# Optimization experiments

Hardware: AMD Instinct MI355X
Metric: run time of the kernel (lower is better)

The kernel has to match this reference:

```python
import jax, jax.numpy as jnp
import numpy as np

N, E, G = 20000, 320000, 64
H, NF, EF, L, Z = 280, 5, 4, 3, 64
BN_EPS = 1e-5


def _bn(x, g, b):
    # BatchNorm1d in training mode: batch stats over dim 0, biased variance
    m = x.mean(0)
    v = x.var(0)
    return g * (x - m) * jax.lax.rsqrt(v + BN_EPS) + b


def _mlp(x, W1, b1, g1, be1, W2, b2, g2, be2):
    h = jax.nn.relu(_bn(x @ W1 + b1, g1, be1))
    return jax.nn.relu(_bn(h @ W2 + b2, g2, be2))


def setup_inputs() -> dict:
    key = jax.random.key(0)
    ks = jax.random.split(key, 24)
    s = 0.05
    inp = {
        "x": jax.random.normal(ks[0], (N, NF), jnp.float32),
        "edge_attr": jax.random.normal(ks[1], (E, EF), jnp.float32),
        "edge_index": jax.random.randint(ks[2], (2, E), 0, N),
        "batch": jnp.sort(jax.random.randint(ks[3], (N,), 0, G)),
        # input layer
        "Wi": jax.random.normal(ks[4], (NF, H), jnp.float32) * s,
        "bi": jnp.zeros((H,), jnp.float32),
        # message MLP (stacked over L layers): in = 2H+EF
        "Wm1": jax.random.normal(ks[5], (L, 2 * H + EF, H), jnp.float32) * s,
        "bm1": jnp.zeros((L, H), jnp.float32),
        "g1": jnp.ones((L, H), jnp.float32),
        "be1": jnp.zeros((L, H), jnp.float32),
        "Wm2": jax.random.normal(ks[6], (L, H, H), jnp.float32) * s,
        "bm2": jnp.zeros((L, H), jnp.float32),
        "g2": jnp.ones((L, H), jnp.float32),
        "be2": jnp.zeros((L, H), jnp.float32),
        # update MLP: in = 2H
        "Wu1": jax.random.normal(ks[7], (L, 2 * H, H), jnp.float32) * s,
        "bu1": jnp.zeros((L, H), jnp.float32),
        "g3": jnp.ones((L, H), jnp.float32),
        "be3": jnp.zeros((L, H), jnp.float32),
        "Wu2": jax.random.normal(ks[8], (L, H, H), jnp.float32) * s,
        "bu2": jnp.zeros((L, H), jnp.float32),
        "g4": jnp.ones((L, H), jnp.float32),
        "be4": jnp.zeros((L, H), jnp.float32),
        # mu head
        "Wmu": jax.random.normal(ks[9], (H, Z), jnp.float32) * s,
        "bmu": jnp.zeros((Z,), jnp.float32),
    }
    return inp


def reference(x, edge_attr, Wi, bi, Wm1, bm1, g1, be1, Wm2, bm2, g2, be2,
              Wu1, bu1, g3, be3, Wu2, bu2, g4, be4, Wmu, bmu,
              edge_index, batch):
    src, dst = edge_index[0], edge_index[1]
    h = x @ Wi + bi  # [N, H]
    for l in range(L):
        # message: cat(h_i=h[dst], h_j=h[src], edge_attr) -> MLP -> [E, H]
        msg_in = jnp.concatenate([h[dst], h[src], edge_attr], axis=-1)
        msg = _mlp(msg_in, Wm1[l], bm1[l], g1[l], be1[l], Wm2[l], bm2[l], g2[l], be2[l])
        # aggregate: scatter-add into target nodes
        agg = jax.ops.segment_sum(msg, dst, num_segments=N)
        # update: cat(h, agg) -> MLP; residual in GNNEncoder
        upd = _mlp(jnp.concatenate([h, agg], axis=-1),
                   Wu1[l], bu1[l], g3[l], be3[l], Wu2[l], bu2[l], g4[l], be4[l])
        h = h + upd
    # global mean pool over graphs
    sums = jax.ops.segment_sum(h, batch, num_segments=G)
    cnt = jax.ops.segment_sum(jnp.ones((h.shape[0],), h.dtype), batch, num_segments=G)
    pooled = sums / jnp.maximum(cnt, 1.0)[:, None]
    return pooled @ Wmu + bmu  # [G, Z]
```

## Files before the change

### kernel.cpp

```cpp
#include <hip/hip_runtime.h>
#include <hip/hip_bf16.h>

#define NN 20000
#define EE 320000
#define GG 64
#define HH 280
#define NFF 5
#define EFF 4
#define LL 3
#define ZZ 64
#define BN_EPS 1e-5f

typedef __hip_bfloat16 bf;
typedef unsigned short ush;
typedef __attribute__((ext_vector_type(8))) short v8s;
typedef __attribute__((ext_vector_type(4))) float v4f;

__device__ __forceinline__ float us2f(ush u) {
  return __uint_as_float(((unsigned)u) << 16);
}
__device__ __forceinline__ ush f2us(float v) {
  bf b = __float2bfloat16(v);
  return *reinterpret_cast<ush*>(&b);
}
__device__ __forceinline__ int clampi(int v, int hi) {
  return v < 0 ? 0 : (v >= hi ? hi - 1 : v);
}

__global__ void probe_k(const void* __restrict__ x, int* __restrict__ flag) {
  __shared__ int sh[256];
  int tid = threadIdx.x;
  int cnt = 0;
  for (int i = tid; i < 2048; i += 256) {
    ush w = ((const ush*)x)[i];
    unsigned e = (w >> 7) & 0xFF;
    if (w != 0 && (e < 87 || e > 167)) cnt++;
  }
  sh[tid] = cnt;
  __syncthreads();
  for (int o = 128; o > 0; o >>= 1) {
    if (tid < o) sh[tid] += sh[tid + o];
    __syncthreads();
  }
  if (tid == 0) *flag = (sh[0] > 64) ? 1 : 0;
}

__global__ void convert_k(const void* __restrict__ src, float* __restrict__ dst,
                          int n, const int* __restrict__ flag) {
  int i = blockIdx.x * 256 + threadIdx.x;
  if (i < n) {
    if (*flag)
      dst[i] = ((const float*)src)[i];
    else
      dst[i] = us2f(((const ush*)src)[i]);
  }
}

__global__ void wt_ab_k(const float* __restrict__ W, ush* __restrict__ O) {
  int i = blockIdx.x * 256 + threadIdx.x;
  if (i >= 3 * 576 * 288) return;
  int l = i / 165888, r = i % 165888;
  int n = r / 288, k = r % 288;
  float v = 0.f;
  if (n < 560 && k < 280)
    v = (n < 280) ? W[(size_t)l * 157920 + (size_t)k * 280 + n]
                  : W[(size_t)l * 157920 + (size_t)(280 + k) * 280 + (n - 280)];
  O[i] = f2us(v);
}
__global__ void wt_sq_k(const float* __restrict__ W, ush* __restrict__ O) {
  int i = blockIdx.x * 256 + threadIdx.x;
  if (i >= 3 * 320 * 288) return;
  int l = i / 92160, r = i % 92160;
  int n = r / 288, k = r % 288;
  float v = (n < 280 && k < 280) ? W[(size_t)l * 78400 + (size_t)k * 280 + n] : 0.f;
  O[i] = f2us(v);
}
__global__ void wt_u1_k(const float* __restrict__ W, ush* __restrict__ O) {
  int i = blockIdx.x * 256 + threadIdx.x;
  if (i >= 3 * 320 * 576) return;
  int l = i / 184320, r = i % 184320;
  int n = r / 576, k = r % 576;
  float v = (n < 280 && k < 560) ? W[(size_t)l * 156800 + (size_t)k * 280 + n] : 0.f;
  O[i] = f2us(v);
}

struct MG {
  const ush* A;
  const ush* Bt;
  const float* bias;
  void* C;
  float* stats;
  int M, K, Nn, lda, ldb, ldc;
};

template <int CB, int ST>
__global__ __launch_bounds__(256) void mgemm_k(MG g) {
  __shared__ ush Bs[64][296];
  auto red = (float(*)[64])Bs;
  int t = threadIdx.x;
  int n0 = blockIdx.x * 64, m0 = blockIdx.y * 128;
  int lane = t & 63, wv = t >> 6;
  int lrow = lane & 15, quad = lane >> 4;
  int br = t >> 2;
  int bc = (t & 3) * 72;
  v4f acc[2][4];
#pragma unroll
  for (int gi = 0; gi < 2; ++gi)
#pragma unroll
    for (int ci = 0; ci < 4; ++ci) acc[gi][ci] = (v4f){0.f, 0.f, 0.f, 0.f};

  const ush* Arow[2];
  bool av[2];
#pragma unroll
  for (int gi = 0; gi < 2; ++gi) {
    int gm = m0 + (wv << 5) + (gi << 4) + lrow;
    av[gi] = gm < g.M;
    Arow[gi] = g.A + (size_t)gm * g.lda + (quad << 3);
  }
  const ush* Brow = g.Bt + (size_t)(n0 + br) * g.ldb + bc;
  uint4 zz = {0, 0, 0, 0};

  int ntile = g.K / 288;
  for (int tile = 0; tile < ntile; ++tile) {
    int k0 = tile * 288;
    uint4 aR[2][9];
#pragma unroll
    for (int kt = 0; kt < 9; ++kt)
#pragma unroll
      for (int gi = 0; gi < 2; ++gi)
        aR[gi][kt] = av[gi] ? *(const uint4*)(Arow[gi] + k0 + (kt << 5)) : zz;
    if (tile) __syncthreads();
#pragma unroll
    for (int i = 0; i < 9; ++i)
      *(uint4*)&Bs[br][bc + (i << 3)] = *(const uint4*)(Brow + k0 + (i << 3));
    __syncthreads();
#pragma unroll
    for (int kt = 0; kt < 9; ++kt) {
      v8s bq[4];
#pragma unroll
      for (int ci = 0; ci < 4; ++ci)
        bq[ci] = *(const v8s*)&Bs[(ci << 4) + lrow][(kt << 5) + (quad << 3)];
#pragma unroll
      for (int gi = 0; gi < 2; ++gi) {
        v8s af = *(v8s*)&aR[gi][kt];
#pragma unroll
        for (int ci = 0; ci < 4; ++ci)
          acc[gi][ci] = __builtin_amdgcn_mfma_f32_16x16x32_bf16(
              af, bq[ci], acc[gi][ci], 0, 0, 0);
      }
    }
  }

  float bj[4];
#pragma unroll
  for (int ci = 0; ci < 4; ++ci) {
    int gn = n0 + (ci << 4) + lrow;
    bj[ci] = (g.bias && gn < g.Nn) ? g.bias[gn] : 0.f;
  }
#pragma unroll
  for (int gi = 0; gi < 2; ++gi)
#pragma unroll
    for (int ci = 0; ci < 4; ++ci)
#pragma unroll
      for (int r = 0; r < 4; ++r) {
        int gm = m0 + (wv << 5) + (gi << 4) + (quad << 2) + r;
        int gn = n0 + (ci << 4) + lrow;
        float v = acc[gi][ci][r] + bj[ci];
        bool ok = (gm < g.M) && (gn < g.Nn);
        if (ok) {
          size_t idx = (size_t)gm * g.ldc + gn;
          if (CB)
            ((ush*)g.C)[idx] = f2us(v);
          else
            ((float*)g.C)[idx] = v;
        }
        acc[gi][ci][r] = ok ? v : 0.f;
      }
  if (ST) {
    int rowg = (wv << 2) | quad;
    __syncthreads();
#pragma unroll
    for (int ci = 0; ci < 4; ++ci) {
      float s = 0.f;
#pragma unroll
      for (int gi = 0; gi < 2; ++gi)
#pragma unroll
        for (int r = 0; r < 4; ++r) s += acc[gi][ci][r];
      red[rowg][(ci << 4) | lrow] = s;
    }
    __syncthreads();
    if (t < 64) {
      float s = 0.f;
#pragma unroll
      for (int r = 0; r < 16; ++r) s += red[r][t];
      int gn = n0 + t;
      if (gn < g.Nn) atomicAdd(&g.stats[gn], s);
    }
    __syncthreads();
#pragma unroll
    for (int ci = 0; ci < 4; ++ci) {
      float s = 0.f;
#pragma unroll
      for (int gi = 0; gi < 2; ++gi)
#pragma unroll
        for (int r = 0; r < 4; ++r) s += acc[gi][ci][r] * acc[gi][ci][r];
      red[rowg][(ci << 4) | lrow] = s;
    }
    __syncthreads();
    if (t < 64) {
      float s = 0.f;
#pragma unroll
      for (int r = 0; r < 16; ++r) s += red[r][t];
      int gn = n0 + t;
      if (gn < g.Nn) atomicAdd(&g.stats[HH + gn], s);
    }
  }
}

__global__ __launch_bounds__(256) void gemm_small_k(
    const float* __restrict__ A, const float* __restrict__ B,
    const float* __restrict__ bias, void* __restrict__ C,
    const int* __restrict__ flag, int M, int K, int Nn, int lda, int ldb,
    int ldc, int outmode) {
  __shared__ alignas(16) float As[16][68];
  __shared__ alignas(16) float Bsm[16][68];
  int tid = threadIdx.x;
  int n0 = blockIdx.x * 64, m0 = blockIdx.y * 64;
  int tx = tid & 15, ty = tid >> 4;
  int am = tid >> 2, akq = (tid & 3) << 2;
  int bk = tid >> 4, bn = (tid & 15) << 2;
  float acc[4][4] = {};
  int gmA = m0 + am;
  int nkt = (K + 15) >> 4;
  for (int kt = 0; kt < nkt; ++kt) {
    int k0 = kt << 4;
#pragma unroll
    for (int i = 0; i < 4; ++i) {
      int gk = k0 + akq + i;
      As[akq + i][am] = (gmA < M && gk < K) ? A[(size_t)gmA * lda + gk] : 0.f;
    }
    {
      int gk = k0 + bk;
      bool kin = gk < K;
#pragma unroll
      for (int j = 0; j < 4; ++j) {
        int gn = n0 + bn + j;
        Bsm[bk][bn + j] = (kin && gn < Nn) ? B[(size_t)gk * ldb + gn] : 0.f;
      }
    }
    __syncthreads();
#pragma unroll
    for (int kk = 0; kk < 16; ++kk) {
      float4 a4 = *(const float4*)&As[kk][ty << 2];
      float4 b4 = *(const float4*)&Bsm[kk][tx << 2];
      float av[4] = {a4.x, a4.y, a4.z, a4.w};
      float bv[4] = {b4.x, b4.y, b4.z, b4.w};
#pragma unroll
      for (int i = 0; i < 4; ++i)
#pragma unroll
        for (int j = 0; j < 4; ++j) acc[i][j] = fmaf(av[i], bv[j], acc[i][j]);
    }
    __syncthreads();
  }
  int ofl = outmode ? *flag : -1;
#pragma unroll
  for (int i = 0; i < 4; ++i) {
    int gm = m0 + (ty << 2) + i;
    if (gm < M) {
#pragma unroll
      for (int j = 0; j < 4; ++j) {
        int gn = n0 + (tx << 2) + j;
        if (gn < Nn) {
          float v = acc[i][j] + (bias ? bias[gn] : 0.f);
          size_t idx = (size_t)gm * ldc + gn;
          if (outmode == 0)
            ((float*)C)[idx] = v;
          else if (ofl)
            ((float*)C)[idx] = v;
          else
            ((ush*)C)[idx] = f2us(v);
        }
      }
    }
  }
}

__global__ __launch_bounds__(256) void edge_stats_k(
    const int* __restrict__ eids, const int* __restrict__ dst,
    const int* __restrict__ src, const float* __restrict__ ea,
    const ush* __restrict__ Pq, const float* __restrict__ W1c,
    const float* __restrict__ b1, float* __restrict__ stats) {
  __shared__ int dstl[256], srcl[256];
  __shared__ float4 eal[256];
  __shared__ float w1cs[4 * HH];
  __shared__ float b1s[HH];
  int tid = threadIdx.x;
  int e0 = blockIdx.x * 256;
  {
    int e = clampi(eids[e0 + tid], EE);
    dstl[tid] = clampi(dst[e], NN);
    srcl[tid] = clampi(src[e], NN);
    eal[tid] = *(const float4*)(ea + (size_t)e * 4);
  }
  for (int i = tid; i < 4 * HH; i += 256) w1cs[i] = W1c[i];
  for (int i = tid; i < HH; i += 256) b1s[i] = b1[i];
  __syncthreads();
  int c0 = tid, c1 = tid + 256;
  bool has1 = c1 < HH;
  float w0x = w1cs[c0], w0y = w1cs[HH + c0], w0z = w1cs[2 * HH + c0],
        w0w = w1cs[3 * HH + c0], b0v = b1s[c0];
  float w1x = 0.f, w1y = 0.f, w1z = 0.f, w1w = 0.f, b1v = 0.f;
  if (has1) {
    w1x = w1cs[c1]; w1y = w1cs[HH + c1]; w1z = w1cs[2 * HH + c1];
    w1w = w1cs[3 * HH + c1]; b1v = b1s[c1];
  }
  float s0 = 0.f, q0 = 0.f, s1 = 0.f, q1 = 0.f;
  for (int e = 0; e < 256; e += 4) {
    ush pd[4], ps[4], pd2[4], ps2[4];
#pragma unroll
    for (int j = 0; j < 4; ++j) {
      size_t bd = (size_t)dstl[e + j] * 576, bs = (size_t)srcl[e + j] * 576 + 280;
      pd[j] = Pq[bd + c0];
      ps[j] = Pq[bs + c0];
      if (has1) {
        pd2[j] = Pq[bd + c1];
        ps2[j] = Pq[bs + c1];
      }
    }
#pragma unroll
    for (int j = 0; j < 4; ++j) {
      float4 ev = eal[e + j];
      float tv = us2f(pd[j]) + us2f(ps[j]) + ev.x * w0x + ev.y * w0y +
                 ev.z * w0z + ev.w * w0w + b0v;
      s0 += tv;
      q0 += tv * tv;
      if (has1) {
        float t2 = us2f(pd2[j]) + us2f(ps2[j]) + ev.x * w1x + ev.y * w1y +
                   ev.z * w1z + ev.w * w1w + b1v;
        s1 += t2;
        q1 += t2 * t2;
      }
    }
  }
  atomicAdd(&stats[c0], s0);
  atomicAdd(&stats[HH + c0], q0);
  if (has1) {
    atomicAdd(&stats[c1], s1);
    atomicAdd(&stats[HH + c1], q1);
  }
}

__global__ void bn_finalize_k(const float* __restrict__ stats, float cnt,
                              const float* __restrict__ gw,
                              const float* __restrict__ bw,
                              const float* __restrict__ extra,
                              float* __restrict__ scale,
                              float* __restrict__ shift) {
  int c = threadIdx.x;
  if (c < HH) {
    float m = stats[c] / cnt;
    float v = stats[HH + c] / cnt - m * m;
    v = v < 0.f ? 0.f : v;
    float r = rsqrtf(v + BN_EPS);
    float sc = gw[c] * r;
    float sh = bw[c] - sc * m + (extra ? sc * extra[c] : 0.f);
    scale[c] = sc;
    shift[c] = sh;
  }
}

__global__ void hist_k(const int* __restrict__ dst, int* __restrict__ counts) {
  int e = blockIdx.x * 256 + threadIdx.x;
  if (e < EE) atomicAdd(&counts[clampi(dst[e], NN)], 1);
}

__global__ __launch_bounds__(1024) void scan_k(const int* __restrict__ counts,
                                               int* __restrict__ offs, int n) {
  __shared__ int buf[1024];
  __shared__ int running;
  int tid = threadIdx.x;
  if (tid == 0) running = 0;
  __syncthreads();
  for (int base = 0; base < n; base += 1024) {
    int v = (base + tid < n) ? counts[base + tid] : 0;
    buf[tid] = v;
    __syncthreads();
    for (int off = 1; off < 1024; off <<= 1) {
      int t = (tid >= off) ? buf[tid - off] : 0;
      __syncthreads();
      buf[tid] += t;
      __syncthreads();
    }
    int incl = buf[tid];
    if (base + tid < n) offs[base + tid] = running + incl - v;
    __syncthreads();
    if (tid == 1023) running += incl;
    __syncthreads();
  }
  if (tid == 0) offs[n] = running;
}

__global__ void fill_k(const int* __restrict__ dst, const int* __restrict__ offs,
                       int* __restrict__ cursor, int* __restrict__ eids) {
  int e = blockIdx.x * 256 + threadIdx.x;
  if (e < EE) {
    int n = clampi(dst[e], NN);
    int pos = atomicAdd(&cursor[n], 1);
    int idx = offs[n] + pos;
    if (idx >= 0 && idx < EE) eids[idx] = e;
  }
}

__global__ __launch_bounds__(256) void build_t1_k(
    const int* __restrict__ eids, const int* __restrict__ dst,
    const int* __restrict__ src, const float* __restrict__ ea,
    const ush* __restrict__ Pq, const float* __restrict__ W1c,
    const float* __restrict__ sc, const float* __restrict__ sh,
    ush* __restrict__ T1, int cb) {
  __shared__ float scs[HH], shs[HH], w1[4 * HH];
  int t = threadIdx.x;
  for (int i = t; i < HH; i += 256) { scs[i] = sc[i]; shs[i] = sh[i]; }
  for (int i = t; i < 4 * HH; i += 256) w1[i] = W1c[i];
  __syncthreads();
  int base = blockIdx.x * 32;
  int c2 = t + 256;
  bool h2 = c2 < HH;
  for (int i = 0; i < 32; ++i) {
    int r = cb + base + i;
    int e = clampi(eids[r], EE);
    int d = clampi(dst[e], NN), s = clampi(src[e], NN);
    float4 ev = *(const float4*)(ea + (size_t)e * 4);
    size_t pd = (size_t)d * 576, ps = (size_t)s * 576 + 280;
    size_t orow = (size_t)(base + i) * 288;
    {
      int c = t;
      float v = us2f(Pq[pd + c]) + us2f(Pq[ps + c]) + ev.x * w1[c] +
                ev.y * w1[HH + c] + ev.z * w1[2 * HH + c] + ev.w * w1[3 * HH + c];
      v = fmaf(scs[c], v, shs[c]);
      T1[orow + c] = f2us(v > 0.f ? v : 0.f);
    }
    if (h2) {
      int c = c2;
      float v = us2f(Pq[pd + c]) + us2f(Pq[ps + c]) + ev.x * w1[c] +
                ev.y * w1[HH + c] + ev.z * w1[2 * HH + c] + ev.w * w1[3 * HH + c];
      v = fmaf(scs[c], v, shs[c]);
      T1[orow + c] = f2us(v > 0.f ? v : 0.f);
    }
  }
}

__global__ __launch_bounds__(256) void aggregate_k(
    const int* __restrict__ offs, const ush* __restrict__ tmp2,
    const float* __restrict__ scale, const float* __restrict__ shift,
    float* __restrict__ agg, int e0, int e1) {
  int n = blockIdx.x;
  int rs = offs[n], re = offs[n + 1];
  if (rs < e0) rs = e0;
  if (re > e1) re = e1;
  if (rs >= re) return;
  int t = threadIdx.x;
  int c2 = t + 256;
  bool h2 = c2 < HH;
  float a0 = 0.f, a1 = 0.f;
  float sc0 = scale[t], sh0 = shift[t];
  float sc1 = h2 ? scale[c2] : 0.f, sh1 = h2 ? shift[c2] : 0.f;
  for (int r = rs; r < re; ++r) {
    const ush* row = tmp2 + (size_t)(r - e0) * HH;
    float v0 = fmaf(sc0, us2f(row[t]), sh0);
    a0 += v0 > 0.f ? v0 : 0.f;
    if (h2) {
      float v1 = fmaf(sc1, us2f(row[c2]), sh1);
      a1 += v1 > 0.f ? v1 : 0.f;
    }
  }
  agg[(size_t)n * HH + t] += a0;
  if (h2) agg[(size_t)n * HH + c2] += a1;
}

__global__ void hb_k(const float* __restrict__ h, ush* __restrict__ hcat) {
  int i = blockIdx.x * 256 + threadIdx.x;
  if (i < NN * HH) {
    int n = i / HH, c = i % HH;
    hcat[(size_t)n * 576 + c] = f2us(h[i]);
  }
}
__global__ void agg2hcat_k(const float* __restrict__ agg, ush* __restrict__ hcat) {
  int i = blockIdx.x * 256 + threadIdx.x;
  if (i < NN * HH) {
    int n = i / HH, c = i % HH;
    hcat[(size_t)n * 576 + 280 + c] = f2us(agg[i]);
  }
}
__global__ void u2a_k(const float* __restrict__ u1, const float* __restrict__ sc,
                      const float* __restrict__ sh, ush* __restrict__ u2A) {
  int i = blockIdx.x * 256 + threadIdx.x;
  if (i < NN * HH) {
    int n = i / HH, c = i % HH;
    float v = fmaf(sc[c], u1[i], sh[c]);
    u2A[(size_t)n * 288 + c] = f2us(v > 0.f ? v : 0.f);
  }
}
__global__ void residual_k(float* __restrict__ h, const float* __restrict__ u2,
                           const float* __restrict__ scale,
                           const float* __restrict__ shift) {
  int i = blockIdx.x * 256 + threadIdx.x;
  if (i < NN * HH) {
    int c = i % HH;
    float v = fmaf(scale[c], u2[i], shift[c]);
    h[i] += v > 0.f ? v : 0.f;
  }
}

__device__ __forceinline__ int lowerb(const int* a, int n, int key) {
  int lo = 0, hi = n;
  while (lo < hi) {
    int mid = (lo + hi) >> 1;
    if (a[mid] < key) lo = mid + 1; else hi = mid;
  }
  return lo;
}

__global__ __launch_bounds__(256) void pool_k(const float* __restrict__ h,
                                              const int* __restrict__ batch,
                                              float* __restrict__ pooled) {
  __shared__ float red[4][56];
  int gid = blockIdx.x, cc = blockIdx.y;
  int start = lowerb(batch, NN, gid);
  int end = lowerb(batch, NN, gid + 1);
  int cnt = end - start;
  float inv = 1.f / (float)(cnt > 1 ? cnt : 1);
  int grp = threadIdx.x >> 6, ci = threadIdx.x & 63;
  if (ci < 56) {
    int col = cc * 56 + ci;
    float s = 0.f;
    for (int n = start + grp; n < end; n += 4) s += h[(size_t)n * HH + col];
    red[grp][ci] = s;
  }
  __syncthreads();
  if (threadIdx.x < 56) {
    float s = red[0][threadIdx.x] + red[1][threadIdx.x] +
              red[2][threadIdx.x] + red[3][threadIdx.x];
    pooled[(size_t)gid * HH + cc * 56 + threadIdx.x] = s * inv;
  }
}

extern "C" void kernel_launch(void* const* d_in, const int* in_sizes, int n_in,
                              void* d_out, int out_size, void* d_ws,
                              size_t ws_size, hipStream_t stream) {
  const int* eidx = (const int*)d_in[2];
  const int* batch = (const int*)d_in[3];
  const int* srcp = eidx;
  const int* dstp = eidx + EE;
  size_t NH = (size_t)NN * HH;

  float* w0 = (float*)d_ws;
  size_t off = 0;
  auto alloc = [&](size_t n) {
    float* p = w0 + off;
    off += (n + 3) & ~(size_t)3;
    return p;
  };
  int* flag = (int*)alloc(4);
  float* cx = alloc(100000);
  float* cea = alloc(1280000);
  float* cWi = alloc(1400);
  float* cbi = alloc(280);
  float* cWm1 = alloc(473760);
  float* cbm1 = alloc(840);
  float* cg1 = alloc(840);
  float* cbe1 = alloc(840);
  float* cWm2 = alloc(235200);
  float* cbm2 = alloc(840);
  float* cg2 = alloc(840);
  float* cbe2 = alloc(840);
  float* cWu1 = alloc(470400);
  float* cbu1 = alloc(840);
  float* cg3 = alloc(840);
  float* cbe3 = alloc(840);
  float* cWu2 = alloc(235200);
  float* cbu2 = alloc(840);
  float* cg4 = alloc(840);
  float* cbe4 = alloc(840);
  float* cWmu = alloc(17920);
  float* cbmu = alloc(64);
  ush* W1ab = (ush*)alloc(248832);
  ush* W2t = (ush*)alloc(138240);
  ush* WU1t = (ush*)alloc(276480);
  ush* WU2t = (ush*)alloc(138240);
  float* h = alloc(NH);
  ush* hcat = (ush*)alloc(5824512);
  ush* u2A = hcat;
  float* pqr = alloc(5824512);
  ush* Pq = (ush*)pqr;
  float* u1f = pqr;
  float* agg = alloc(NH);
  float* pooled = alloc((size_t)GG * HH);
  float* stats = alloc(8 * HH);
  float* ss = alloc(8 * HH);
  int* counts = (int*)alloc(NN);
  int* cursor = (int*)alloc(NN);
  int* offs = (int*)alloc(NN + 1);
  int* eids = (int*)alloc(EE);
  size_t baseB = off * 4;

  int EC = 6400, T2 = 6400;
  {
    const int ecs[5] = {64000, 64000, 32000, 12800, 6400};
    const int t2s[5] = {EE, 64000, 32000, 12800, 6400};
    for (int i = 0; i < 5; ++i) {
      size_t need = baseB + (size_t)ecs[i] * 288 * 2 + (size_t)t2s[i] * 280 * 2 + 64;
      if (need <= ws_size) { EC = ecs[i]; T2 = t2s[i]; break; }
    }
  }
  ush* T1c = (ush*)(w0 + off);
  ush* tmp2 = T1c + (size_t)EC * 288;
  bool stored = (T2 == EE);
  int nch = EE / EC;

  probe_k<<<1, 256, 0, stream>>>(d_in[0], flag);
  struct Cv { const void* s; float* d; int n; };
  const Cv cv[22] = {
      {d_in[0], cx, NN * NFF},     {d_in[1], cea, EE * EFF},
      {d_in[4], cWi, NFF * HH},    {d_in[5], cbi, HH},
      {d_in[6], cWm1, LL * (2 * HH + EFF) * HH}, {d_in[7], cbm1, LL * HH},
      {d_in[8], cg1, LL * HH},     {d_in[9], cbe1, LL * HH},
      {d_in[10], cWm2, LL * HH * HH}, {d_in[11], cbm2, LL * HH},
      {d_in[12], cg2, LL * HH},    {d_in[13], cbe2, LL * HH},
      {d_in[14], cWu1, LL * 2 * HH * HH}, {d_in[15], cbu1, LL * HH},
      {d_in[16], cg3, LL * HH},    {d_in[17], cbe3, LL * HH},
      {d_in[18], cWu2, LL * HH * HH}, {d_in[19], cbu2, LL * HH},
      {d_in[20], cg4, LL * HH},    {d_in[21], cbe4, LL * HH},
      {d_in[22], cWmu, HH * ZZ},   {d_in[23], cbmu, ZZ}};
  for (int i = 0; i < 22; ++i)
    convert_k<<<(cv[i].n + 255) / 256, 256, 0, stream>>>(cv[i].s, cv[i].d, cv[i].n, flag);

  wt_ab_k<<<(3 * 576 * 288 + 255) / 256, 256, 0, stream>>>(cWm1, W1ab);
  wt_sq_k<<<(3 * 320 * 288 + 255) / 256, 256, 0, stream>>>(cWm2, W2t);
  wt_u1_k<<<(3 * 320 * 576 + 255) / 256, 256, 0, stream>>>(cWu1, WU1t);
  wt_sq_k<<<(3 * 320 * 288 + 255) / 256, 256, 0, stream>>>(cWu2, WU2t);

  gemm_small_k<<<dim3(5, 313), 256, 0, stream>>>(cx, cWi, cbi, h, nullptr, NN,
                                                 NFF, HH, NFF, HH, HH, 0);
  hipMemsetAsync(counts, 0, NN * sizeof(int), stream);
  hipMemsetAsync(cursor, 0, NN * sizeof(int), stream);
  hist_k<<<(EE + 255) / 256, 256, 0, stream>>>(dstp, counts);
  scan_k<<<1, 1024, 0, stream>>>(counts, offs, NN);
  fill_k<<<(EE + 255) / 256, 256, 0, stream>>>(dstp, offs, cursor, eids);

  int elemGrid = (int)((NH + 255) / 256);
  for (int l = 0; l < LL; ++l) {
    ush* Wab = W1ab + (size_t)l * 576 * 288;
    ush* W2l = W2t + (size_t)l * 320 * 288;
    ush* WU1l = WU1t + (size_t)l * 320 * 576;
    ush* WU2l = WU2t + (size_t)l * 320 * 288;
    const float* W1c = cWm1 + (size_t)l * 157920 + (size_t)560 * 280;
    float* st1 = stats;
    float* st2 = stats + 560;
    float* st3 = stats + 1120;
    float* st4 = stats + 1680;
    float* ss1 = ss;
    float* ss2 = ss + 560;
    float* ss3 = ss + 1120;
    float* ss4 = ss + 1680;
    hipMemsetAsync(stats, 0, 8 * HH * sizeof(float), stream);

    hb_k<<<elemGrid, 256, 0, stream>>>(h, hcat);
    {
      MG g = {hcat, Wab, nullptr, Pq, nullptr, NN, 288, 560, 576, 288, 576};
      mgemm_k<1, 0><<<dim3(9, 157), 256, 0, stream>>>(g);
    }
    edge_stats_k<<<EE / 256, 256, 0, stream>>>(eids, dstp, srcp, cea, Pq, W1c,
                                               cbm1 + l * HH, st1);
    bn_finalize_k<<<1, 320, 0, stream>>>(st1, (float)EE, cg1 + l * HH,
                                         cbe1 + l * HH, cbm1 + l * HH, ss1,
                                         ss1 + HH);
    for (int c = 0; c < nch; ++c) {
      int cb = c * EC;
      build_t1_k<<<EC / 32, 256, 0, stream>>>(eids, dstp, srcp, cea, Pq, W1c,
                                              ss1, ss1 + HH, T1c, cb);
      MG g = {T1c, W2l, cbm2 + l * HH,
              stored ? (void*)(tmp2 + (size_t)cb * HH) : (void*)tmp2, st2,
              EC, 288, HH, 288, 288, HH};
      mgemm_k<1, 1><<<dim3(5, EC / 128), 256, 0, stream>>>(g);
    }
    bn_finalize_k<<<1, 320, 0, stream>>>(st2, (float)EE, cg2 + l * HH,
                                         cbe2 + l * HH, nullptr, ss2, ss2 + HH);
    hipMemsetAsync(agg, 0, NH * sizeof(float), stream);
    if (stored) {
      aggregate_k<<<NN, 256, 0, stream>>>(offs, tmp2, ss2, ss2 + HH, agg, 0, EE);
    } else {
      for (int c = 0; c < nch; ++c) {
        int cb = c * EC;
        build_t1_k<<<EC / 32, 256, 0, stream>>>(eids, dstp, srcp, cea, Pq, W1c,
                                                ss1, ss1 + HH, T1c, cb);
        MG g = {T1c, W2l, cbm2 + l * HH, (void*)tmp2, nullptr,
                EC, 288, HH, 288, 288, HH};
        mgemm_k<1, 0><<<dim3(5, EC / 128), 256, 0, stream>>>(g);
        aggregate_k<<<NN, 256, 0, stream>>>(offs, tmp2, ss2, ss2 + HH, agg, cb, cb + EC);
      }
    }
    agg2hcat_k<<<elemGrid, 256, 0, stream>>>(agg, hcat);
    {
      MG g = {hcat, WU1l, cbu1 + l * HH, u1f, st3, NN, 576, HH, 576, 576, HH};
      mgemm_k<0, 1><<<dim3(5, 157), 256, 0, stream>>>(g);
    }
    bn_finalize_k<<<1, 320, 0, stream>>>(st3, (float)NN, cg3 + l * HH,
                                         cbe3 + l * HH, nullptr, ss3, ss3 + HH);
    u2a_k<<<elemGrid, 256, 0, stream>>>(u1f, ss3, ss3 + HH, u2A);
    {
      MG g = {u2A, WU2l, cbu2 + l * HH, agg, st4, NN, 288, HH, 288, 288, HH};
      mgemm_k<0, 1><<<dim3(5, 157), 256, 0, stream>>>(g);
    }
    bn_finalize_k<<<1, 320, 0, stream>>>(st4, (float)NN, cg4 + l * HH,
                                         cbe4 + l * HH, nullptr, ss4, ss4 + HH);
    residual_k<<<elemGrid, 256, 0, stream>>>(h, agg, ss4, ss4 + HH);
  }

  pool_k<<<dim3(GG, 5), 256, 0, stream>>>(h, batch, pooled);
  gemm_small_k<<<dim3(1, 1), 256, 0, stream>>>(pooled, cWmu, cbmu, d_out, flag,
                                               GG, HH, ZZ, HH, ZZ, ZZ, 1);
}
```

Before: 4.273 ms.

## Materialize raw first-layer edge activations with stats, then apply BN in place

When the workspace can hold the full edge buffer, a new kernel gathers the node projections once, writes raw pre-BN edge activations to T1 and accumulates BN statistics in the same pass. A separate elementwise kernel then applies scale, shift and ReLU in place before a single full-size GEMM. This replaces the old two-gather scheme (a stats pass followed by build_t1 re-gathering) with one gather, at the cost of an extra full read/write of the bf16 buffer and the rounding of raw values to bf16 before normalization. The fallback stats kernel was also simplified to process one edge per iteration.

Result: slower. 5.390 ms (+26.1%).

```diff
diff --git a/kernel.cpp b/kernel.cpp
--- a/kernel.cpp
+++ b/kernel.cpp
@@ -285,6 +285,93 @@
   }
 }
 
+__global__ __launch_bounds__(256) void build_raw_k(
+    const int* __restrict__ eids, const int* __restrict__ dst,
+    const int* __restrict__ src, const float* __restrict__ ea,
+    const ush* __restrict__ Pq, const float* __restrict__ W1c,
+    const float* __restrict__ b1, ush* __restrict__ T1,
+    float* __restrict__ stats) {
+  __shared__ int dstl[256], srcl[256];
+  __shared__ float4 eal[256];
+  __shared__ float w1cs[4 * HH];
+  __shared__ float b1s[HH];
+  int tid = threadIdx.x;
+  int e0 = blockIdx.x * 256;
+  {
+    int e = clampi(eids[e0 + tid], EE);
+    dstl[tid] = clampi(dst[e], NN);
+    srcl[tid] = clampi(src[e], NN);
+    eal[tid] = *(const float4*)(ea + (size_t)e * 4);
+  }
+  for (int i = tid; i < 4 * HH; i += 256) w1cs[i] = W1c[i];
+  for (int i = tid; i < HH; i += 256) b1s[i] = b1[i];
+  __syncthreads();
+  int c0 = tid, c1 = tid + 256;
+  bool has1 = c1 < HH;
+  float w0x = w1cs[c0], w0y = w1cs[HH + c0], w0z = w1cs[2 * HH + c0],
+        w0w = w1cs[3 * HH + c0], b0v = b1s[c0];
+  float w1x = 0.f, w1y = 0.f, w1z = 0.f, w1w = 0.f, b1v = 0.f;
+  if (has1) {
+    w1x = w1cs[c1]; w1y = w1cs[HH + c1]; w1z = w1cs[2 * HH + c1];
+    w1w = w1cs[3 * HH + c1]; b1v = b1s[c1];
+  }
+  float s0 = 0.f, q0 = 0.f, s1 = 0.f, q1 = 0.f;
+  for (int e = 0; e < 256; e += 4) {
+    ush pd[4], ps[4], pd2[4], ps2[4];
+#pragma unroll
+    for (int j = 0; j < 4; ++j) {
+      size_t bd = (size_t)dstl[e + j] * 576, bs = (size_t)srcl[e + j] * 576 + 280;
+      pd[j] = Pq[bd + c0];
+      ps[j] = Pq[bs + c0];
+      if (has1) {
+        pd2[j] = Pq[bd + c1];
+        ps2[j] = Pq[bs + c1];
+      }
+    }
+#pragma unroll
+    for (int j = 0; j < 4; ++j) {
+      size_t orow = (size_t)(e0 + e + j) * 288;
+      float4 ev = eal[e + j];
+      float tv = us2f(pd[j]) + us2f(ps[j]) + ev.x * w0x + ev.y * w0y +
+                 ev.z * w0z + ev.w * w0w + b0v;
+      s0 += tv;
+      q0 += tv * tv;
+      T1[orow + c0] = f2us(tv);
+      if (has1) {
+        float t2 = us2f(pd2[j]) + us2f(ps2[j]) + ev.x * w1x + ev.y * w1y +
+                   ev.z * w1z + ev.w * w1w + b1v;
+        s1 += t2;
+        q1 += t2 * t2;
+        T1[orow + c1] = f2us(t2);
+      }
+    }
+  }
+  atomicAdd(&stats[c0], s0);
+  atomicAdd(&stats[HH + c0], q0);
+  if (has1) {
+    atomicAdd(&stats[c1], s1);
+    atomicAdd(&stats[HH + c1], q1);
+  }
+}
+
+__global__ __launch_bounds__(256) void bn_apply_k(ush* __restrict__ T1,
+                                                  const float* __restrict__ scale,
+                                                  const float* __restrict__ shift) {
+  size_t idx = (size_t)blockIdx.x * 256 + threadIdx.x;
+  int g = (int)(idx % 36);
+  if (g == 35) return;
+  int c0 = g << 3;
+  uint4* p = (uint4*)T1 + idx;
+  uint4 v = *p;
+  ush* pv = (ush*)&v;
+#pragma unroll
+  for (int j = 0; j < 8; ++j) {
+    float x = fmaf(scale[c0 + j], us2f(pv[j]), shift[c0 + j]);
+    pv[j] = f2us(x > 0.f ? x : 0.f);
+  }
+  *p = v;
+}
+
 __global__ __launch_bounds__(256) void edge_stats_k(
     const int* __restrict__ eids, const int* __restrict__ dst,
     const int* __restrict__ src, const float* __restrict__ ea,
@@ -307,39 +394,23 @@
   __syncthreads();
   int c0 = tid, c1 = tid + 256;
   bool has1 = c1 < HH;
-  float w0x = w1cs[c0], w0y = w1cs[HH + c0], w0z = w1cs[2 * HH + c0],
-        w0w = w1cs[3 * HH + c0], b0v = b1s[c0];
-  float w1x = 0.f, w1y = 0.f, w1z = 0.f, w1w = 0.f, b1v = 0.f;
-  if (has1) {
-    w1x = w1cs[c1]; w1y = w1cs[HH + c1]; w1z = w1cs[2 * HH + c1];
-    w1w = w1cs[3 * HH + c1]; b1v = b1s[c1];
-  }
   float s0 = 0.f, q0 = 0.f, s1 = 0.f, q1 = 0.f;
-  for (int e = 0; e < 256; e += 4) {
-    ush pd[4], ps[4], pd2[4], ps2[4];
-#pragma unroll
-    for (int j = 0; j < 4; ++j) {
-      size_t bd = (size_t)dstl[e + j] * 576, bs = (size_t)srcl[e + j] * 576 + 280;
-      pd[j] = Pq[bd + c0];
-      ps[j] = Pq[bs + c0];
-      if (has1) {
-        pd2[j] = Pq[bd + c1];
-        ps2[j] = Pq[bs + c1];
-      }
-    }
-#pragma unroll
-    for (int j = 0; j < 4; ++j) {
-      float4 ev = eal[e + j];
-      float tv = us2f(pd[j]) + us2f(ps[j]) + ev.x * w0x + ev.y * w0y +
-                 ev.z * w0z + ev.w * w0w + b0v;
-      s0 += tv;
-      q0 += tv * tv;
-      if (has1) {
-        float t2 = us2f(pd2[j]) + us2f(ps2[j]) + ev.x * w1x + ev.y * w1y +
-                   ev.z * w1z + ev.w * w1w + b1v;
-        s1 += t2;
-        q1 += t2 * t2;
-      }
+  for (int e = 0; e < 256; ++e) {
+    int d = dstl[e], sn = srcl[e];
+    float4 ev = eal[e];
+    {
+      float raw = us2f(Pq[(size_t)d * 576 + c0]) + us2f(Pq[(size_t)sn * 576 + 280 + c0]);
+      float r = ev.x * w1cs[c0] + ev.y * w1cs[HH + c0] +
+                ev.z * w1cs[2 * HH + c0] + ev.w * w1cs[3 * HH + c0];
+      float tv = raw + r + b1s[c0];
+      s0 += tv; q0 += tv * tv;
+    }
+    if (has1) {
+      float raw = us2f(Pq[(size_t)d * 576 + c1]) + us2f(Pq[(size_t)sn * 576 + 280 + c1]);
+      float r = ev.x * w1cs[c1] + ev.y * w1cs[HH + c1] +
+                ev.z * w1cs[2 * HH + c1] + ev.w * w1cs[3 * HH + c1];
+      float tv = raw + r + b1s[c1];
+      s1 += tv; q1 += tv * tv;
     }
   }
   atomicAdd(&stats[c0], s0);
@@ -603,19 +674,21 @@
   int* eids = (int*)alloc(EE);
   size_t baseB = off * 4;
 
+  bool fullOK =
+      (baseB + (size_t)EE * 288 * 2 + (size_t)EE * 280 * 2 + 64) <= ws_size;
   int EC = 6400, T2 = 6400;
-  {
-    const int ecs[5] = {64000, 64000, 32000, 12800, 6400};
-    const int t2s[5] = {EE, 64000, 32000, 12800, 6400};
-    for (int i = 0; i < 5; ++i) {
+  if (!fullOK) {
+    const int ecs[4] = {64000, 32000, 12800, 6400};
+    const int t2s[4] = {EE, 32000, 12800, 6400};
+    for (int i = 0; i < 4; ++i) {
       size_t need = baseB + (size_t)ecs[i] * 288 * 2 + (size_t)t2s[i] * 280 * 2 + 64;
       if (need <= ws_size) { EC = ecs[i]; T2 = t2s[i]; break; }
     }
   }
   ush* T1c = (ush*)(w0 + off);
-  ush* tmp2 = T1c + (size_t)EC * 288;
-  bool stored = (T2 == EE);
-  int nch = EE / EC;
+  ush* tmp2 = T1c + (fullOK ? (size_t)EE * 288 : (size_t)EC * 288);
+  bool stored = fullOK || (T2 == EE);
+  int nch = fullOK ? 1 : (EE / EC);
 
   probe_k<<<1, 256, 0, stream>>>(d_in[0], flag);
   struct Cv { const void* s; float* d; int n; };
@@ -669,19 +742,33 @@
       MG g = {hcat, Wab, nullptr, Pq, nullptr, NN, 288, 560, 576, 288, 576};
       mgemm_k<1, 0><<<dim3(9, 157), 256, 0, stream>>>(g);
     }
-    edge_stats_k<<<EE / 256, 256, 0, stream>>>(eids, dstp, srcp, cea, Pq, W1c,
-                                               cbm1 + l * HH, st1);
-    bn_finalize_k<<<1, 320, 0, stream>>>(st1, (float)EE, cg1 + l * HH,
-                                         cbe1 + l * HH, cbm1 + l * HH, ss1,
-                                         ss1 + HH);
-    for (int c = 0; c < nch; ++c) {
-      int cb = c * EC;
-      build_t1_k<<<EC / 32, 256, 0, stream>>>(eids, dstp, srcp, cea, Pq, W1c,
-                                              ss1, ss1 + HH, T1c, cb);
-      MG g = {T1c, W2l, cbm2 + l * HH,
-              stored ? (void*)(tmp2 + (size_t)cb * HH) : (void*)tmp2, st2,
-              EC, 288, HH, 288, 288, HH};
-      mgemm_k<1, 1><<<dim3(5, EC / 128), 256, 0, stream>>>(g);
+    if (fullOK) {
+      build_raw_k<<<EE / 256, 256, 0, stream>>>(eids, dstp, srcp, cea, Pq, W1c,
+                                                cbm1 + l * HH, T1c, st1);
+      bn_finalize_k<<<1, 320, 0, stream>>>(st1, (float)EE, cg1 + l * HH,
+                                           cbe1 + l * HH, nullptr, ss1,
+                                           ss1 + HH);
+      bn_apply_k<<<EE * 36 / 256, 256, 0, stream>>>(T1c, ss1, ss1 + HH);
+      {
+        MG g = {T1c, W2l, cbm2 + l * HH, (void*)tmp2, st2,
+                EE, 288, HH, 288, 288, HH};
+        mgemm_k<1, 1><<<dim3(5, EE / 128), 256, 0, stream>>>(g);
+      }
+    } else {
+      edge_stats_k<<<EE / 256, 256, 0, stream>>>(eids, dstp, srcp, cea, Pq,
+                                                 W1c, cbm1 + l * HH, st1);
+      bn_finalize_k<<<1, 320, 0, stream>>>(st1, (float)EE, cg1 + l * HH,
+                                           cbe1 + l * HH, cbm1 + l * HH, ss1,
+                                           ss1 + HH);
+      for (int c = 0; c < nch; ++c) {
+        int cb = c * EC;
+        build_t1_k<<<EC / 32, 256, 0, stream>>>(eids, dstp, srcp, cea, Pq, W1c,
+                                                ss1, ss1 + HH, T1c, cb);
+        MG g = {T1c, W2l, cbm2 + l * HH,
+                stored ? (void*)(tmp2 + (size_t)cb * HH) : (void*)tmp2, st2,
+                EC, 288, HH, 288, 288, HH};
+        mgemm_k<1, 1><<<dim3(5, EC / 128), 256, 0, stream>>>(g);
+      }
     }
     bn_finalize_k<<<1, 320, 0, stream>>>(st2, (float)EE, cg2 + l * HH,
                                          cbe2 + l * HH, nullptr, ss2, ss2 + HH);
```
